# Optimization experiments

Measured on AMD Instinct MI355X. Metric: run time of the kernel, lower is better.

The kernel has to match this reference:

```python
import jax, jax.numpy as jnp
import numpy as np

B, C, H, W = 4, 512, 128, 128
CQ = C // 8


def setup_inputs() -> dict:
    key = jax.random.key(0)
    ks = jax.random.split(key, 8)
    s = 0.05
    return {
        "x": jax.random.normal(ks[0], (B, C, H, W), jnp.float32),
        "Wq": jax.random.normal(ks[1], (CQ, C), jnp.float32) * s,
        "bq": jax.random.normal(ks[2], (CQ,), jnp.float32) * s,
        "Wk": jax.random.normal(ks[3], (CQ, C), jnp.float32) * s,
        "bk": jax.random.normal(ks[4], (CQ,), jnp.float32) * s,
        "Wv": jax.random.normal(ks[5], (C, C), jnp.float32) * s,
        "bv": jax.random.normal(ks[6], (C,), jnp.float32) * s,
        "gamma": jax.random.uniform(ks[7], (1,), jnp.float32),
    }


def reference(x, Wq, bq, Wk, bk, Wv, bv, gamma):
    # 1x1 convs are channel GEMMs
    q = jnp.einsum('oc,bchw->bohw', Wq, x) + bq[None, :, None, None]  # [B,CQ,H,W]
    k = jnp.einsum('oc,bchw->bohw', Wk, x) + bk[None, :, None, None]  # [B,CQ,H,W]
    v = jnp.einsum('oc,bchw->bohw', Wv, x) + bv[None, :, None, None]  # [B,C,H,W]

    h = x.shape[2]
    # column (height-axis) attention energy: [B,H,W,H], masked on i==h
    energy_H = jnp.einsum('bchw,bciw->bhwi', q, k)
    diag = jnp.eye(h, dtype=bool)[:, None, :]  # [H,1,H] broadcast over b,w
    energy_H = jnp.where(diag, -jnp.inf, energy_H)
    # row (width-axis) attention energy: [B,H,W,W]
    energy_W = jnp.einsum('bchw,bchj->bhwj', q, k)

    attn = jax.nn.softmax(jnp.concatenate([energy_H, energy_W], axis=-1), axis=-1)
    attn_H, attn_W = attn[..., :h], attn[..., h:]

    out = jnp.einsum('bciw,bhwi->bchw', v, attn_H)
    out = out + jnp.einsum('bchj,bhwj->bchw', v, attn_W)
    return gamma[0] * out + x
```

## Files before the change

kernel.cpp:

```cpp
#include <hip/hip_runtime.h>
#include <hip/hip_bf16.h>
#include <math.h>

typedef unsigned short u16;

#define BB 4
#define CC 512
#define HH 128
#define WW 128
#define PP (HH*WW)

#define NEG_BIG (-3.0e38f)

typedef float f32x4 __attribute__((ext_vector_type(4)));
typedef __bf16 bf16x8 __attribute__((ext_vector_type(8)));

__device__ __forceinline__ float bf2f(u16 u) {
    union { unsigned int i; float f; } v; v.i = ((unsigned int)u) << 16; return v.f;
}
__device__ __forceinline__ u16 f2bf(float f) {
    __hip_bfloat16 h = __float2bfloat16(f);
    u16 u; __builtin_memcpy(&u, &h, 2); return u;
}

template<bool F32>
__device__ __forceinline__ float ldg(const void* p, size_t i) {
    if (F32) return ((const float*)p)[i];
    return bf2f(((const u16*)p)[i]);
}

__device__ __forceinline__ void gl2lds16(const void* g, void* l) {
    __builtin_amdgcn_global_load_lds(
        (const __attribute__((address_space(1))) unsigned int*)g,
        (__attribute__((address_space(3))) unsigned int*)l,
        16, 0, 0);
}

__global__ __launch_bounds__(256) void detect_kernel(const void* x, int* flag)
{
    const int t = threadIdx.x;
    const unsigned int* w = (const unsigned int*)x;
    int cnt = 0;
#pragma unroll
    for (int s = 0; s < 16; s++) {
        unsigned int v = w[t * 16 + s];
        int e = (v >> 7) & 0xFF;
        cnt += (e >= 100 && e < 132) ? 1 : 0;
    }
    __shared__ int sh[256];
    sh[t] = cnt;
    __syncthreads();
    for (int o = 128; o; o >>= 1) {
        if (t < o) sh[t] += sh[t + o];
        __syncthreads();
    }
    if (t == 0) *flag = (sh[0] < 2048) ? 1 : 0;
}

template<bool F32>
__device__ __forceinline__ void wconv_body(
    const void* Wq, const void* bq, const void* Wk, const void* bk,
    const void* Wv, const void* bv,
    u16* __restrict__ Wh, u16* __restrict__ Wl, float* __restrict__ bcat)
{
    const int o = blockIdx.x;
    const int t = threadIdx.x;
#pragma unroll
    for (int s = 0; s < 2; s++) {
        int c = t + s * 256;
        float v;
        if (o < 64)       v = ldg<F32>(Wq, (size_t)o * CC + c);
        else if (o < 128) v = ldg<F32>(Wk, (size_t)(o - 64) * CC + c);
        else              v = ldg<F32>(Wv, (size_t)(o - 128) * CC + c);
        u16 h = f2bf(v);
        Wh[(size_t)o * CC + c] = h;
        Wl[(size_t)o * CC + c] = f2bf(v - bf2f(h));
    }
    if (t == 0) {
        bcat[o] = (o < 64) ? ldg<F32>(bq, o)
                : (o < 128) ? ldg<F32>(bk, o - 64)
                : ldg<F32>(bv, o - 128);
    }
}

__global__ __launch_bounds__(256) void wconv_kernel(
    const void* Wq, const void* bq, const void* Wk, const void* bk,
    const void* Wv, const void* bv, const int* __restrict__ dflag,
    u16* Wh, u16* Wl, float* bcat)
{
    if (*dflag) wconv_body<true >(Wq, bq, Wk, bk, Wv, bv, Wh, Wl, bcat);
    else        wconv_body<false>(Wq, bq, Wk, bk, Wv, bv, Wh, Wl, bcat);
}

template<bool F32>
__device__ __forceinline__ void trans_body(
    const void* __restrict__ x, u16* __restrict__ xh, u16* __restrict__ xl,
    float (*T)[65])
{
    const int t = threadIdx.x;
    const int p0 = blockIdx.x * 64;
    const int c0 = blockIdx.y * 64;
    {
        const int pp = t & 63;
        const int cb = t >> 6;
#pragma unroll
        for (int s = 0; s < 16; s++) {
            int cc = cb * 16 + s;
            T[cc][pp] = ldg<F32>(x, (size_t)(c0 + cc) * PP + p0 + pp);
        }
    }
    __syncthreads();
    {
        const int pr = t >> 2;
        const int cb = (t & 3) * 16;
        u16 hi[16], lo[16];
#pragma unroll
        for (int j = 0; j < 16; j++) {
            float v = T[cb + j][pr];
            u16 h = f2bf(v);
            hi[j] = h;
            lo[j] = f2bf(v - bf2f(h));
        }
        size_t base = (size_t)(p0 + pr) * 512 + c0 + cb;
#pragma unroll
        for (int s = 0; s < 4; s++) {
            *(ushort4*)(xh + base + s * 4) = *(ushort4*)(hi + s * 4);
            *(ushort4*)(xl + base + s * 4) = *(ushort4*)(lo + s * 4);
        }
    }
}

__global__ __launch_bounds__(256) void trans_kernel(
    const void* x_f32, const void* x_b16, const int* __restrict__ dflag,
    u16* xh, u16* xl)
{
    __shared__ float T[64][65];
    if (*dflag) trans_body<true >(x_f32, xh, xl, T);
    else        trans_body<false>(x_b16, xh, xl, T);
}

#define FRAG_OFFS_A(arr)                                        \
    int arr[4];                                                 \
    _Pragma("unroll")                                           \
    for (int ii = 0; ii < 4; ii++) {                            \
        int row = wr * 64 + ii * 16 + fr;                       \
        arr[ii] = row * 32 + ((fq ^ (row & 3)) * 8);            \
    }
#define FRAG_OFFS_B(arr)                                        \
    int arr[2];                                                 \
    _Pragma("unroll")                                           \
    for (int ii = 0; ii < 2; ii++) {                            \
        int row = wc * 32 + ii * 16 + fr;                       \
        arr[ii] = row * 32 + ((fq ^ (row & 3)) * 8);            \
    }

__global__ __launch_bounds__(512) void projmm_kernel(
    const u16* __restrict__ xT_hi, const u16* __restrict__ xT_lo,
    const u16* __restrict__ W_hi,  const u16* __restrict__ W_lo,
    const float* __restrict__ bcat,
    u16* __restrict__ q2, u16* __restrict__ k2, u16* __restrict__ v_c)
{
    __shared__ __align__(16) u16 Asl[128 * 32];
    __shared__ __align__(16) u16 Bsl[128 * 32];
    const int t = threadIdx.x;
    const int lane = t & 63, wid = t >> 6;
    const int wr = wid >> 2, wc = wid & 3;
    const int fr = lane & 15, fq = lane >> 4;
    const int p0 = blockIdx.x * 128;
    const int o0 = blockIdx.y * 128;
    const int KTOT = (blockIdx.y == 0) ? 1536 : 512;

    f32x4 acc[4][2];
#pragma unroll
    for (int i = 0; i < 4; i++)
#pragma unroll
        for (int j = 0; j < 2; j++) acc[i][j] = (f32x4){0.f, 0.f, 0.f, 0.f};

    const int srow = wid * 16 + (lane >> 2);
    const int kch  = (lane & 3) ^ ((lane >> 2) & 3);
    const size_t gA0 = (size_t)(p0 + srow) * 512 + kch * 8;
    const size_t gB0 = (size_t)(o0 + srow) * 512 + kch * 8;
    u16* ldsA = Asl + wid * 512;
    u16* ldsB = Bsl + wid * 512;

    FRAG_OFFS_A(aoff)
    FRAG_OFFS_B(boff)

    for (int k0 = 0; k0 < KTOT; k0 += 32) {
        const int rg = k0 >> 9;
        const int kc = k0 & 511;
        const u16* xs   = (rg == 2) ? xT_lo : xT_hi;
        const u16* wsrc = (rg == 1) ? W_lo  : W_hi;
        gl2lds16(xs + gA0 + kc, ldsA);
        gl2lds16(wsrc + gB0 + kc, ldsB);
        __syncthreads();

        bf16x8 av[4], bv2[2];
#pragma unroll
        for (int mi = 0; mi < 4; mi++) av[mi] = *(const bf16x8*)(Asl + aoff[mi]);
#pragma unroll
        for (int ni = 0; ni < 2; ni++) bv2[ni] = *(const bf16x8*)(Bsl + boff[ni]);
#pragma unroll
        for (int mi = 0; mi < 4; mi++)
#pragma unroll
            for (int ni = 0; ni < 2; ni++)
                acc[mi][ni] = __builtin_amdgcn_mfma_f32_16x16x32_bf16(
                    av[mi], bv2[ni], acc[mi][ni], 0, 0, 0);
        __syncthreads();
    }

#pragma unroll
    for (int ni = 0; ni < 2; ni++) {
        const int o = o0 + wc * 32 + ni * 16 + fr;
        const float bb = bcat[o];
        if (o < 64) {
#pragma unroll
            for (int mi = 0; mi < 4; mi++) {
                const int pb = p0 + wr * 64 + mi * 16 + fq * 4;
#pragma unroll
                for (int r = 0; r < 4; r++) {
                    float val = acc[mi][ni][r] + bb;
                    u16 hi = f2bf(val);
                    q2[(size_t)(pb + r) * 128 + o]      = hi;
                    q2[(size_t)(pb + r) * 128 + 64 + o] = f2bf(val - bf2f(hi));
                }
            }
        } else if (o < 128) {
            const int oc = o - 64;
#pragma unroll
            for (int mi = 0; mi < 4; mi++) {
                const int pb = p0 + wr * 64 + mi * 16 + fq * 4;
#pragma unroll
                for (int r = 0; r < 4; r++) {
                    float val = acc[mi][ni][r] + bb;
                    u16 hi = f2bf(val);
                    k2[(size_t)(pb + r) * 128 + oc]      = hi;
                    k2[(size_t)(pb + r) * 128 + 64 + oc] = f2bf(val - bf2f(hi));
                }
            }
        } else {
            const int ch = o - 128;
#pragma unroll
            for (int mi = 0; mi < 4; mi++) {
                const int pb = p0 + wr * 64 + mi * 16 + fq * 4;
                ushort4 u = { f2bf(acc[mi][ni][0] + bb), f2bf(acc[mi][ni][1] + bb),
                              f2bf(acc[mi][ni][2] + bb), f2bf(acc[mi][ni][3] + bb) };
                *(ushort4*)(v_c + (size_t)ch * PP + pb) = u;
            }
        }
    }
}

__global__ __launch_bounds__(256) void vtrans_kernel(
    const u16* __restrict__ v_c, u16* __restrict__ v_a)
{
    const int c  = blockIdx.x;
    const int w0 = blockIdx.y * 64;
    const int t  = threadIdx.x;
    __shared__ __align__(16) u16 T[64 * 132];
#pragma unroll
    for (int s = 0; s < 4; s++) {
        const int h  = (t >> 3) + s * 32;
        const int wl = (t & 7) * 8;
        const u16* src = v_c + (size_t)c * PP + h * 128 + w0 + wl;
        ushort4 a0 = *(const ushort4*)(src);
        ushort4 a1 = *(const ushort4*)(src + 4);
        T[(wl + 0) * 132 + h] = a0.x; T[(wl + 1) * 132 + h] = a0.y;
        T[(wl + 2) * 132 + h] = a0.z; T[(wl + 3) * 132 + h] = a0.w;
        T[(wl + 4) * 132 + h] = a1.x; T[(wl + 5) * 132 + h] = a1.y;
        T[(wl + 6) * 132 + h] = a1.z; T[(wl + 7) * 132 + h] = a1.w;
    }
    __syncthreads();
#pragma unroll
    for (int s = 0; s < 4; s++) {
        const int wl = (t >> 4) + s * 16;
        const int hh = (t & 15) * 8;
        ushort4 b0 = *(const ushort4*)(T + wl * 132 + hh);
        ushort4 b1 = *(const ushort4*)(T + wl * 132 + hh + 4);
        ushort4* dp = (ushort4*)(v_a + (size_t)c * PP + (size_t)(w0 + wl) * 128 + hh);
        dp[0] = b0; dp[1] = b1;
    }
}

__device__ __forceinline__ void mm128_core8(
    const u16* __restrict__ baseA, size_t sA,
    const u16* __restrict__ baseB, size_t sB,
    u16* Asl, u16* Bsl, int lane, int wid,
    const int* aoff, const int* boff, f32x4 (*acc)[2])
{
    const int srow = wid * 16 + (lane >> 2);
    const int kch  = (lane & 3) ^ ((lane >> 2) & 3);
    const u16* gA = baseA + (size_t)srow * sA + kch * 8;
    const u16* gB = baseB + (size_t)srow * sB + kch * 8;
    u16* ldsA = Asl + wid * 512;
    u16* ldsB = Bsl + wid * 512;
    for (int k0 = 0; k0 < 128; k0 += 32) {
        gl2lds16(gA + k0, ldsA);
        gl2lds16(gB + k0, ldsB);
        __syncthreads();
        bf16x8 av[4], bv2[2];
#pragma unroll
        for (int mi = 0; mi < 4; mi++) av[mi] = *(const bf16x8*)(Asl + aoff[mi]);
#pragma unroll
        for (int ni = 0; ni < 2; ni++) bv2[ni] = *(const bf16x8*)(Bsl + boff[ni]);
#pragma unroll
        for (int mi = 0; mi < 4; mi++)
#pragma unroll
            for (int ni = 0; ni < 2; ni++)
                acc[mi][ni] = __builtin_amdgcn_mfma_f32_16x16x32_bf16(
                    av[mi], bv2[ni], acc[mi][ni], 0, 0, 0);
        __syncthreads();
    }
}

__global__ __launch_bounds__(512) void energy_mm_kernel(
    const u16* __restrict__ q2, const u16* __restrict__ k2,
    float* __restrict__ attn_f)
{
    __shared__ __align__(16) u16 Asl[128 * 32];
    __shared__ __align__(16) u16 Bsl[128 * 32];
    const int t = threadIdx.x;
    const int lane = t & 63, wid = t >> 6;
    const int wr = wid >> 2, wc = wid & 3;
    const int fr = lane & 15, fq = lane >> 4;
    const int isW = blockIdx.y;
    const int fx  = blockIdx.x;

    const size_t sA   = isW ? 128 : (size_t)128 * 128;
    const size_t base = isW ? (size_t)fx * 128 * 128 : (size_t)fx * 128;

    f32x4 acc[4][2];
#pragma unroll
    for (int i = 0; i < 4; i++)
#pragma unroll
        for (int j = 0; j < 2; j++) acc[i][j] = (f32x4){0.f, 0.f, 0.f, 0.f};

    const int srow = wid * 16 + (lane >> 2);
    const int kch  = (lane & 3) ^ ((lane >> 2) & 3);
    const u16* gA = q2 + base + (size_t)srow * sA + kch * 8;
    const u16* gB = k2 + base + (size_t)srow * sA + kch * 8;
    u16* ldsA = Asl + wid * 512;
    u16* ldsB = Bsl + wid * 512;

    FRAG_OFFS_A(aoff)
    FRAG_OFFS_B(boff)

    const int AK[6] = {0, 32, 0, 32, 64, 96};
    const int BK[6] = {0, 32, 64, 96, 0, 32};
#pragma unroll
    for (int s = 0; s < 6; s++) {
        gl2lds16(gA + AK[s], ldsA);
        gl2lds16(gB + BK[s], ldsB);
        __syncthreads();
        bf16x8 av[4], bv2[2];
#pragma unroll
        for (int mi = 0; mi < 4; mi++) av[mi] = *(const bf16x8*)(Asl + aoff[mi]);
#pragma unroll
        for (int ni = 0; ni < 2; ni++) bv2[ni] = *(const bf16x8*)(Bsl + boff[ni]);
#pragma unroll
        for (int mi = 0; mi < 4; mi++)
#pragma unroll
            for (int ni = 0; ni < 2; ni++)
                acc[mi][ni] = __builtin_amdgcn_mfma_f32_16x16x32_bf16(
                    av[mi], bv2[ni], acc[mi][ni], 0, 0, 0);
        __syncthreads();
    }

#pragma unroll
    for (int ni = 0; ni < 2; ni++) {
        const int cn = wc * 32 + ni * 16 + fr;
#pragma unroll
        for (int mi = 0; mi < 4; mi++) {
            const int rm0 = wr * 64 + mi * 16 + fq * 4;
#pragma unroll
            for (int r = 0; r < 4; r++) {
                const int rm = rm0 + r;
                const size_t prow = isW ? ((size_t)fx * 128 + rm)
                                        : ((size_t)rm * 128 + fx);
                float vv = acc[mi][ni][r];
                if (!isW && cn == rm) vv = NEG_BIG;
                attn_f[prow * 256 + (size_t)isW * 128 + cn] = vv;
            }
        }
    }
}

__global__ __launch_bounds__(512) void aggA_mm_kernel(
    const u16* __restrict__ v_a, const u16* __restrict__ attn_b,
    u16* __restrict__ out_t)
{
    __shared__ __align__(16) u16 Asl[128 * 32];
    __shared__ __align__(16) u16 Bsl[128 * 32];
    __shared__ __align__(16) u16 Dst[128 * 132];
    const int t = threadIdx.x;
    const int lane = t & 63, wid = t >> 6;
    const int wr = wid >> 2, wc = wid & 3;
    const int fr = lane & 15, fq = lane >> 4;
    const int c0 = blockIdx.x * 128;
    const int w  = blockIdx.y;

    f32x4 acc[4][2];
#pragma unroll
    for (int i = 0; i < 4; i++)
#pragma unroll
        for (int j = 0; j < 2; j++) acc[i][j] = (f32x4){0.f, 0.f, 0.f, 0.f};

    FRAG_OFFS_A(aoff)
    FRAG_OFFS_B(boff)

    mm128_core8(attn_b + (size_t)w * 256, (size_t)128 * 256,
                v_a + (size_t)c0 * PP + (size_t)w * 128, (size_t)PP,
                Asl, Bsl, lane, wid, aoff, boff, acc);

#pragma unroll
    for (int mi = 0; mi < 4; mi++)
#pragma unroll
        for (int ni = 0; ni < 2; ni++) {
            const int c = wc * 32 + ni * 16 + fr;
#pragma unroll
            for (int r = 0; r < 4; r++) {
                const int h = wr * 64 + mi * 16 + fq * 4 + r;
                Dst[h * 132 + c] = f2bf(acc[mi][ni][r]);
            }
        }
    __syncthreads();
#pragma unroll
    for (int s = 0; s < 4; s++) {
        const int h = s * 32 + (t >> 4);
        const int c = (t & 15) * 8;
        ushort4 a0 = *(const ushort4*)(Dst + h * 132 + c);
        ushort4 a1 = *(const ushort4*)(Dst + h * 132 + c + 4);
        ushort4* dp = (ushort4*)(out_t + (size_t)(h * WW + w) * 512 + c0 + c);
        dp[0] = a0; dp[1] = a1;
    }
}

template<bool F32>
__device__ __forceinline__ void aggB_mm_body(
    const u16* __restrict__ v_c, const u16* __restrict__ attn_b,
    const u16* __restrict__ out_t, const void* __restrict__ x,
    const void* __restrict__ gamma, void* __restrict__ out,
    u16* Asl, u16* Bsl, char* epi)
{
    const int t = threadIdx.x;
    const int lane = t & 63, wid = t >> 6;
    const int wr = wid >> 2, wc = wid & 3;
    const int fr = lane & 15, fq = lane >> 4;
    const int c0 = blockIdx.x * 128;
    const int h  = blockIdx.y;

    f32x4 acc[4][2];
#pragma unroll
    for (int i = 0; i < 4; i++)
#pragma unroll
        for (int j = 0; j < 2; j++) acc[i][j] = (f32x4){0.f, 0.f, 0.f, 0.f};

    FRAG_OFFS_A(aoff)
    FRAG_OFFS_B(boff)

    mm128_core8(attn_b + (size_t)h * 128 * 256 + 128, (size_t)256,
                v_c + (size_t)c0 * PP + (size_t)h * 128, (size_t)PP,
                Asl, Bsl, lane, wid, aoff, boff, acc);

    u16* OAs = (u16*)epi;
#pragma unroll
    for (int s = 0; s < 4; s++) {
        const int wrow = s * 32 + (t >> 4);
        const int c = (t & 15) * 8;
        const u16* sp = out_t + (size_t)(h * WW + wrow) * 512 + c0 + c;
        ushort4 a0 = *(const ushort4*)(sp);
        ushort4 a1 = *(const ushort4*)(sp + 4);
        *(ushort4*)(OAs + wrow * 136 + c)     = a0;
        *(ushort4*)(OAs + wrow * 136 + c + 4) = a1;
    }
    __syncthreads();
#pragma unroll
    for (int mi = 0; mi < 4; mi++)
#pragma unroll
        for (int ni = 0; ni < 2; ni++) {
            const int c = wc * 32 + ni * 16 + fr;
#pragma unroll
            for (int r = 0; r < 4; r++) {
                const int ww = wr * 64 + mi * 16 + fq * 4 + r;
                acc[mi][ni][r] += bf2f(OAs[ww * 136 + c]);
            }
        }
    __syncthreads();

    const float g = ldg<F32>(gamma, 0);
    float* DstF = (float*)epi;
#pragma unroll
    for (int half = 0; half < 2; half++) {
        if ((wc >> 1) == half) {
#pragma unroll
            for (int mi = 0; mi < 4; mi++)
#pragma unroll
                for (int ni = 0; ni < 2; ni++) {
                    const int cl = (wc & 1) * 32 + ni * 16 + fr;
                    const int w0 = wr * 64 + mi * 16 + fq * 4;
                    f32x4 vv = acc[mi][ni];
                    *(f32x4*)(DstF + cl * 132 + w0) = vv;
                }
        }
        __syncthreads();
#pragma unroll
        for (int s = 0; s < 4; s++) {
            const int e  = s * 2048 + t * 4;
            const int cl = e >> 7;
            const int wq = e & 127;
            f32x4 vv = *(const f32x4*)(DstF + cl * 132 + wq);
            const size_t base = (size_t)(c0 + half * 64 + cl) * PP + h * 128 + wq;
            float r0 = g * vv[0] + ldg<F32>(x, base + 0);
            float r1 = g * vv[1] + ldg<F32>(x, base + 1);
            float r2 = g * vv[2] + ldg<F32>(x, base + 2);
            float r3 = g * vv[3] + ldg<F32>(x, base + 3);
            if (F32) {
                *(float4*)((float*)out + base) = make_float4(r0, r1, r2, r3);
            } else {
                ushort4 o = { f2bf(r0), f2bf(r1), f2bf(r2), f2bf(r3) };
                *(ushort4*)((u16*)out + base) = o;
            }
        }
        __syncthreads();
    }
}

__global__ __launch_bounds__(512) void aggB_mm_kernel(
    const u16* v_c, const u16* attn_b, const u16* out_t,
    const void* x_f32, const void* x_b16, const void* gamma,
    const int* __restrict__ dflag, void* out_f32, void* out_b16)
{
    __shared__ __align__(16) u16 Asl[128 * 32];
    __shared__ __align__(16) u16 Bsl[128 * 32];
    __shared__ __align__(16) char epi[128 * 136 * 2];
    if (*dflag)
        aggB_mm_body<true >(v_c, attn_b, out_t, x_f32, gamma, out_f32, Asl, Bsl, epi);
    else
        aggB_mm_body<false>(v_c, attn_b, out_t, x_b16, gamma, out_b16, Asl, Bsl, epi);
}

__global__ __launch_bounds__(256) void softmax_kernel(
    const float* __restrict__ attn_f, u16* __restrict__ attn_b)
{
    const int wave = threadIdx.x >> 6, lane = threadIdx.x & 63;
    const size_t row = (size_t)blockIdx.x * 4 + wave;
    const float* rp = attn_f + row * 256;
    float4 v = ((const float4*)rp)[lane];
    v.x = isfinite(v.x) ? v.x : NEG_BIG;
    v.y = isfinite(v.y) ? v.y : NEG_BIG;
    v.z = isfinite(v.z) ? v.z : NEG_BIG;
    v.w = isfinite(v.w) ? v.w : NEG_BIG;
    float m = fmaxf(fmaxf(v.x, v.y), fmaxf(v.z, v.w));
#pragma unroll
    for (int off = 32; off; off >>= 1) m = fmaxf(m, __shfl_xor(m, off));
    float e0 = __expf(v.x - m), e1 = __expf(v.y - m);
    float e2 = __expf(v.z - m), e3 = __expf(v.w - m);
    float s = e0 + e1 + e2 + e3;
#pragma unroll
    for (int off = 32; off; off >>= 1) s += __shfl_xor(s, off);
    float inv = 1.0f / s;
    ushort4 u = { f2bf(e0 * inv), f2bf(e1 * inv), f2bf(e2 * inv), f2bf(e3 * inv) };
    ((ushort4*)(attn_b + row * 256))[lane] = u;
}

extern "C" void kernel_launch(void* const* d_in, const int* in_sizes, int n_in,
                              void* d_out, int out_size, void* d_ws, size_t ws_size,
                              hipStream_t stream)
{
    const void* x     = d_in[0];
    const void* Wq    = d_in[1];
    const void* bq    = d_in[2];
    const void* Wk    = d_in[3];
    const void* bk    = d_in[4];
    const void* Wv    = d_in[5];
    const void* bv    = d_in[6];
    const void* gamma = d_in[7];

    char* ws = (char*)d_ws;
    int*   dflag = (int*)ws;
    float* bcat  = (float*)(ws + 256);
    size_t off = 4096;
    u16* W_hi = (u16*)(ws + off); off += (size_t)640 * 512 * 2;
    u16* W_lo = (u16*)(ws + off); off += (size_t)640 * 512 * 2;
    u16* q2   = (u16*)(ws + off); off += (size_t)PP * 128 * 2;
    u16* k2   = (u16*)(ws + off); off += (size_t)PP * 128 * 2;
    u16* v_c   = (u16*)(ws + off);  off += (size_t)PP * 512 * 2;
    u16* xT_hi = (u16*)(ws + off);  off += (size_t)PP * 512 * 2;
    u16* xT_lo = (u16*)(ws + off);  off += (size_t)PP * 512 * 2;
    float* attn_f = (float*)xT_hi;
    u16*   v_a    = (u16*)xT_hi;
    u16*   attn_b = (u16*)q2;
    u16*   out_t  = (u16*)xT_lo;

    detect_kernel<<<dim3(1), 256, 0, stream>>>(x, dflag);
    wconv_kernel<<<dim3(640), 256, 0, stream>>>(
        Wq, bq, Wk, bk, Wv, bv, dflag, W_hi, W_lo, bcat);

    for (int b = 0; b < BB; b++) {
        const void* x_f = (const void*)((const float*)x + (size_t)b * CC * PP);
        const void* x_h = (const void*)((const u16*)x   + (size_t)b * CC * PP);
        void* o_f = (void*)((float*)d_out + (size_t)b * CC * PP);
        void* o_h = (void*)((u16*)d_out   + (size_t)b * CC * PP);
        trans_kernel<<<dim3(PP / 64, CC / 64), 256, 0, stream>>>(
            x_f, x_h, dflag, xT_hi, xT_lo);
        projmm_kernel<<<dim3(PP / 128, 5), 512, 0, stream>>>(
            xT_hi, xT_lo, W_hi, W_lo, bcat, q2, k2, v_c);
        energy_mm_kernel<<<dim3(128, 2), 512, 0, stream>>>(q2, k2, attn_f);
        softmax_kernel<<<dim3(PP / 4), 256, 0, stream>>>(attn_f, attn_b);
        vtrans_kernel<<<dim3(CC, 2), 256, 0, stream>>>(v_c, v_a);
        aggA_mm_kernel<<<dim3(4, WW), 512, 0, stream>>>(v_a, attn_b, out_t);
        aggB_mm_kernel<<<dim3(4, HH), 512, 0, stream>>>(
            v_c, attn_b, out_t, x_f, x_h, gamma, dflag, o_f, o_h);
    }
}
```

Baseline: 650.4 us.

## Double K-tile depth to 64 in all MFMA GEMMs and alias LDS buffers

All bf16 MFMA GEMM loops (projection, energy, both aggregations) now stage 64-wide K slices per iteration instead of 32. This halves the number of barrier pairs and load phases and widens the XOR swizzle to 8 chunks. The aggregation kernels also overlay the A/B staging buffers with the epilogue buffer, so the extra tile size does not raise LDS use and occupancy can be kept. The cost is more LDS per block in the projection and energy kernels, and the aliasing depends on the barrier that already follows the main loop.

```diff
diff --git a/kernel.cpp b/kernel.cpp
--- a/kernel.cpp
+++ b/kernel.cpp
@@ -139,19 +139,23 @@
     else        trans_body<false>(x_b16, xh, xl, T);
 }
 
-#define FRAG_OFFS_A(arr)                                        \
-    int arr[4];                                                 \
-    _Pragma("unroll")                                           \
-    for (int ii = 0; ii < 4; ii++) {                            \
-        int row = wr * 64 + ii * 16 + fr;                       \
-        arr[ii] = row * 32 + ((fq ^ (row & 3)) * 8);            \
-    }
-#define FRAG_OFFS_B(arr)                                        \
-    int arr[2];                                                 \
-    _Pragma("unroll")                                           \
-    for (int ii = 0; ii < 2; ii++) {                            \
-        int row = wc * 32 + ii * 16 + fr;                       \
-        arr[ii] = row * 32 + ((fq ^ (row & 3)) * 8);            \
+#define FRAG_OFFS_A64(arr)                                          \
+    int arr[4][2];                                                  \
+    _Pragma("unroll")                                               \
+    for (int ii = 0; ii < 4; ii++) {                                \
+        int row = wr * 64 + ii * 16 + fr;                           \
+        _Pragma("unroll")                                           \
+        for (int hf = 0; hf < 2; hf++)                              \
+            arr[ii][hf] = row * 64 + (((hf * 4 + fq) ^ (row & 7)) * 8); \
+    }
+#define FRAG_OFFS_B64(arr)                                          \
+    int arr[2][2];                                                  \
+    _Pragma("unroll")                                               \
+    for (int ii = 0; ii < 2; ii++) {                                \
+        int row = wc * 32 + ii * 16 + fr;                           \
+        _Pragma("unroll")                                           \
+        for (int hf = 0; hf < 2; hf++)                              \
+            arr[ii][hf] = row * 64 + (((hf * 4 + fq) ^ (row & 7)) * 8); \
     }
 
 __global__ __launch_bounds__(512) void projmm_kernel(
@@ -160,8 +164,8 @@
     const float* __restrict__ bcat,
     u16* __restrict__ q2, u16* __restrict__ k2, u16* __restrict__ v_c)
 {
-    __shared__ __align__(16) u16 Asl[128 * 32];
-    __shared__ __align__(16) u16 Bsl[128 * 32];
+    __shared__ __align__(16) u16 Asl[128 * 64];
+    __shared__ __align__(16) u16 Bsl[128 * 64];
     const int t = threadIdx.x;
     const int lane = t & 63, wid = t >> 6;
     const int wr = wid >> 2, wc = wid & 3;
@@ -176,36 +180,42 @@
 #pragma unroll
         for (int j = 0; j < 2; j++) acc[i][j] = (f32x4){0.f, 0.f, 0.f, 0.f};
 
-    const int srow = wid * 16 + (lane >> 2);
-    const int kch  = (lane & 3) ^ ((lane >> 2) & 3);
-    const size_t gA0 = (size_t)(p0 + srow) * 512 + kch * 8;
-    const size_t gB0 = (size_t)(o0 + srow) * 512 + kch * 8;
-    u16* ldsA = Asl + wid * 512;
-    u16* ldsB = Bsl + wid * 512;
-
-    FRAG_OFFS_A(aoff)
-    FRAG_OFFS_B(boff)
-
-    for (int k0 = 0; k0 < KTOT; k0 += 32) {
+    const int srow_l = lane >> 3;
+    const int gk     = ((lane & 7) ^ srow_l) * 8;
+    const int row0   = wid * 16 + srow_l;
+    const size_t gA0 = (size_t)(p0 + row0) * 512 + gk;
+    const size_t gB0 = (size_t)(o0 + row0) * 512 + gk;
+    u16* ldsA = Asl + wid * 1024;
+    u16* ldsB = Bsl + wid * 1024;
+
+    FRAG_OFFS_A64(aoff)
+    FRAG_OFFS_B64(boff)
+
+    for (int k0 = 0; k0 < KTOT; k0 += 64) {
         const int rg = k0 >> 9;
         const int kc = k0 & 511;
         const u16* xs   = (rg == 2) ? xT_lo : xT_hi;
         const u16* wsrc = (rg == 1) ? W_lo  : W_hi;
-        gl2lds16(xs + gA0 + kc, ldsA);
-        gl2lds16(wsrc + gB0 + kc, ldsB);
-        __syncthreads();
-
-        bf16x8 av[4], bv2[2];
-#pragma unroll
-        for (int mi = 0; mi < 4; mi++) av[mi] = *(const bf16x8*)(Asl + aoff[mi]);
-#pragma unroll
-        for (int ni = 0; ni < 2; ni++) bv2[ni] = *(const bf16x8*)(Bsl + boff[ni]);
-#pragma unroll
-        for (int mi = 0; mi < 4; mi++)
-#pragma unroll
-            for (int ni = 0; ni < 2; ni++)
-                acc[mi][ni] = __builtin_amdgcn_mfma_f32_16x16x32_bf16(
-                    av[mi], bv2[ni], acc[mi][ni], 0, 0, 0);
+        gl2lds16(xs + gA0 + kc,            ldsA);
+        gl2lds16(xs + gA0 + 8 * 512 + kc,  ldsA + 512);
+        gl2lds16(wsrc + gB0 + kc,           ldsB);
+        gl2lds16(wsrc + gB0 + 8 * 512 + kc, ldsB + 512);
+        __syncthreads();
+
+#pragma unroll
+        for (int hf = 0; hf < 2; hf++) {
+            bf16x8 av[4], bv2[2];
+#pragma unroll
+            for (int mi = 0; mi < 4; mi++) av[mi] = *(const bf16x8*)(Asl + aoff[mi][hf]);
+#pragma unroll
+            for (int ni = 0; ni < 2; ni++) bv2[ni] = *(const bf16x8*)(Bsl + boff[ni][hf]);
+#pragma unroll
+            for (int mi = 0; mi < 4; mi++)
+#pragma unroll
+                for (int ni = 0; ni < 2; ni++)
+                    acc[mi][ni] = __builtin_amdgcn_mfma_f32_16x16x32_bf16(
+                        av[mi], bv2[ni], acc[mi][ni], 0, 0, 0);
+        }
         __syncthreads();
     }
 
@@ -286,29 +296,35 @@
     const u16* __restrict__ baseA, size_t sA,
     const u16* __restrict__ baseB, size_t sB,
     u16* Asl, u16* Bsl, int lane, int wid,
-    const int* aoff, const int* boff, f32x4 (*acc)[2])
-{
-    const int srow = wid * 16 + (lane >> 2);
-    const int kch  = (lane & 3) ^ ((lane >> 2) & 3);
-    const u16* gA = baseA + (size_t)srow * sA + kch * 8;
-    const u16* gB = baseB + (size_t)srow * sB + kch * 8;
-    u16* ldsA = Asl + wid * 512;
-    u16* ldsB = Bsl + wid * 512;
-    for (int k0 = 0; k0 < 128; k0 += 32) {
-        gl2lds16(gA + k0, ldsA);
-        gl2lds16(gB + k0, ldsB);
-        __syncthreads();
-        bf16x8 av[4], bv2[2];
-#pragma unroll
-        for (int mi = 0; mi < 4; mi++) av[mi] = *(const bf16x8*)(Asl + aoff[mi]);
-#pragma unroll
-        for (int ni = 0; ni < 2; ni++) bv2[ni] = *(const bf16x8*)(Bsl + boff[ni]);
-#pragma unroll
-        for (int mi = 0; mi < 4; mi++)
-#pragma unroll
-            for (int ni = 0; ni < 2; ni++)
-                acc[mi][ni] = __builtin_amdgcn_mfma_f32_16x16x32_bf16(
-                    av[mi], bv2[ni], acc[mi][ni], 0, 0, 0);
+    const int (*aoff)[2], const int (*boff)[2], f32x4 (*acc)[2])
+{
+    const int srow_l = lane >> 3;
+    const int gk     = ((lane & 7) ^ srow_l) * 8;
+    const int row0   = wid * 16 + srow_l;
+    const u16* gA = baseA + (size_t)row0 * sA + gk;
+    const u16* gB = baseB + (size_t)row0 * sB + gk;
+    u16* ldsA = Asl + wid * 1024;
+    u16* ldsB = Bsl + wid * 1024;
+    for (int k0 = 0; k0 < 128; k0 += 64) {
+        gl2lds16(gA + k0,           ldsA);
+        gl2lds16(gA + 8 * sA + k0,  ldsA + 512);
+        gl2lds16(gB + k0,           ldsB);
+        gl2lds16(gB + 8 * sB + k0,  ldsB + 512);
+        __syncthreads();
+#pragma unroll
+        for (int hf = 0; hf < 2; hf++) {
+            bf16x8 av[4], bv2[2];
+#pragma unroll
+            for (int mi = 0; mi < 4; mi++) av[mi] = *(const bf16x8*)(Asl + aoff[mi][hf]);
+#pragma unroll
+            for (int ni = 0; ni < 2; ni++) bv2[ni] = *(const bf16x8*)(Bsl + boff[ni][hf]);
+#pragma unroll
+            for (int mi = 0; mi < 4; mi++)
+#pragma unroll
+                for (int ni = 0; ni < 2; ni++)
+                    acc[mi][ni] = __builtin_amdgcn_mfma_f32_16x16x32_bf16(
+                        av[mi], bv2[ni], acc[mi][ni], 0, 0, 0);
+        }
         __syncthreads();
     }
 }
@@ -317,8 +333,8 @@
     const u16* __restrict__ q2, const u16* __restrict__ k2,
     float* __restrict__ attn_f)
 {
-    __shared__ __align__(16) u16 Asl[128 * 32];
-    __shared__ __align__(16) u16 Bsl[128 * 32];
+    __shared__ __align__(16) u16 Asl[128 * 64];
+    __shared__ __align__(16) u16 Bsl[128 * 64];
     const int t = threadIdx.x;
     const int lane = t & 63, wid = t >> 6;
     const int wr = wid >> 2, wc = wid & 3;
@@ -335,34 +351,40 @@
 #pragma unroll
         for (int j = 0; j < 2; j++) acc[i][j] = (f32x4){0.f, 0.f, 0.f, 0.f};
 
-    const int srow = wid * 16 + (lane >> 2);
-    const int kch  = (lane & 3) ^ ((lane >> 2) & 3);
-    const u16* gA = q2 + base + (size_t)srow * sA + kch * 8;
-    const u16* gB = k2 + base + (size_t)srow * sA + kch * 8;
-    u16* ldsA = Asl + wid * 512;
-    u16* ldsB = Bsl + wid * 512;
-
-    FRAG_OFFS_A(aoff)
-    FRAG_OFFS_B(boff)
-
-    const int AK[6] = {0, 32, 0, 32, 64, 96};
-    const int BK[6] = {0, 32, 64, 96, 0, 32};
-#pragma unroll
-    for (int s = 0; s < 6; s++) {
-        gl2lds16(gA + AK[s], ldsA);
-        gl2lds16(gB + BK[s], ldsB);
-        __syncthreads();
-        bf16x8 av[4], bv2[2];
-#pragma unroll
-        for (int mi = 0; mi < 4; mi++) av[mi] = *(const bf16x8*)(Asl + aoff[mi]);
-#pragma unroll
-        for (int ni = 0; ni < 2; ni++) bv2[ni] = *(const bf16x8*)(Bsl + boff[ni]);
-#pragma unroll
-        for (int mi = 0; mi < 4; mi++)
-#pragma unroll
-            for (int ni = 0; ni < 2; ni++)
-                acc[mi][ni] = __builtin_amdgcn_mfma_f32_16x16x32_bf16(
-                    av[mi], bv2[ni], acc[mi][ni], 0, 0, 0);
+    const int srow_l = lane >> 3;
+    const int gk     = ((lane & 7) ^ srow_l) * 8;
+    const int row0   = wid * 16 + srow_l;
+    const u16* gA = q2 + base + (size_t)row0 * sA + gk;
+    const u16* gB = k2 + base + (size_t)row0 * sA + gk;
+    u16* ldsA = Asl + wid * 1024;
+    u16* ldsB = Bsl + wid * 1024;
+
+    FRAG_OFFS_A64(aoff)
+    FRAG_OFFS_B64(boff)
+
+    const int AO[3] = {0, 0, 64};
+    const int BO[3] = {0, 64, 0};
+#pragma unroll
+    for (int s = 0; s < 3; s++) {
+        gl2lds16(gA + AO[s],           ldsA);
+        gl2lds16(gA + 8 * sA + AO[s],  ldsA + 512);
+        gl2lds16(gB + BO[s],           ldsB);
+        gl2lds16(gB + 8 * sA + BO[s],  ldsB + 512);
+        __syncthreads();
+#pragma unroll
+        for (int hf = 0; hf < 2; hf++) {
+            bf16x8 av[4], bv2[2];
+#pragma unroll
+            for (int mi = 0; mi < 4; mi++) av[mi] = *(const bf16x8*)(Asl + aoff[mi][hf]);
+#pragma unroll
+            for (int ni = 0; ni < 2; ni++) bv2[ni] = *(const bf16x8*)(Bsl + boff[ni][hf]);
+#pragma unroll
+            for (int mi = 0; mi < 4; mi++)
+#pragma unroll
+                for (int ni = 0; ni < 2; ni++)
+                    acc[mi][ni] = __builtin_amdgcn_mfma_f32_16x16x32_bf16(
+                        av[mi], bv2[ni], acc[mi][ni], 0, 0, 0);
+        }
         __syncthreads();
     }
 
@@ -389,9 +411,10 @@
     const u16* __restrict__ v_a, const u16* __restrict__ attn_b,
     u16* __restrict__ out_t)
 {
-    __shared__ __align__(16) u16 Asl[128 * 32];
-    __shared__ __align__(16) u16 Bsl[128 * 32];
-    __shared__ __align__(16) u16 Dst[128 * 132];
+    __shared__ __align__(16) char smem[128 * 132 * 2];
+    u16* Asl = (u16*)smem;
+    u16* Bsl = (u16*)(smem + 128 * 64 * 2);
+    u16* Dst = (u16*)smem;
     const int t = threadIdx.x;
     const int lane = t & 63, wid = t >> 6;
     const int wr = wid >> 2, wc = wid & 3;
@@ -405,8 +428,8 @@
 #pragma unroll
         for (int j = 0; j < 2; j++) acc[i][j] = (f32x4){0.f, 0.f, 0.f, 0.f};
 
-    FRAG_OFFS_A(aoff)
-    FRAG_OFFS_B(boff)
+    FRAG_OFFS_A64(aoff)
+    FRAG_OFFS_B64(boff)
 
     mm128_core8(attn_b + (size_t)w * 256, (size_t)128 * 256,
                 v_a + (size_t)c0 * PP + (size_t)w * 128, (size_t)PP,
@@ -440,8 +463,11 @@
     const u16* __restrict__ v_c, const u16* __restrict__ attn_b,
     const u16* __restrict__ out_t, const void* __restrict__ x,
     const void* __restrict__ gamma, void* __restrict__ out,
-    u16* Asl, u16* Bsl, char* epi)
-{
+    char* smem)
+{
+    u16* Asl = (u16*)smem;
+    u16* Bsl = (u16*)(smem + 128 * 64 * 2);
+    char* epi = smem;
     const int t = threadIdx.x;
     const int lane = t & 63, wid = t >> 6;
     const int wr = wid >> 2, wc = wid & 3;
@@ -455,8 +481,8 @@
 #pragma unroll
         for (int j = 0; j < 2; j++) acc[i][j] = (f32x4){0.f, 0.f, 0.f, 0.f};
 
-    FRAG_OFFS_A(aoff)
-    FRAG_OFFS_B(boff)
+    FRAG_OFFS_A64(aoff)
+    FRAG_OFFS_B64(boff)
 
     mm128_core8(attn_b + (size_t)h * 128 * 256 + 128, (size_t)256,
                 v_c + (size_t)c0 * PP + (size_t)h * 128, (size_t)PP,
@@ -530,13 +556,11 @@
     const void* x_f32, const void* x_b16, const void* gamma,
     const int* __restrict__ dflag, void* out_f32, void* out_b16)
 {
-    __shared__ __align__(16) u16 Asl[128 * 32];
-    __shared__ __align__(16) u16 Bsl[128 * 32];
-    __shared__ __align__(16) char epi[128 * 136 * 2];
+    __shared__ __align__(16) char smem[128 * 136 * 2];
     if (*dflag)
-        aggB_mm_body<true >(v_c, attn_b, out_t, x_f32, gamma, out_f32, Asl, Bsl, epi);
+        aggB_mm_body<true >(v_c, attn_b, out_t, x_f32, gamma, out_f32, smem);
     else
-        aggB_mm_body<false>(v_c, attn_b, out_t, x_b16, gamma, out_b16, Asl, Bsl, epi);
+        aggB_mm_body<false>(v_c, attn_b, out_t, x_b16, gamma, out_b16, smem);
 }
 
 __global__ __launch_bounds__(256) void softmax_kernel(
```

After: 608.6 us. 1.07x faster.
